# Performance work log

Hardware: AMD Instinct MI355X
Metric: run time of the kernel (lower is better)

The kernel has to match this reference:

```python
import jax, jax.numpy as jnp
import numpy as np
from jax import lax

EMB, HDIM, OBS_LEN = 64, 64, 8
BATCH, NSCENES, SCENE = 32768, 4096, 8
SEQ_LEN = 12


def setup_inputs() -> dict:
    key = jax.random.key(0)
    ks = jax.random.split(key, 16)
    obs_traj = jax.random.normal(ks[0], (OBS_LEN, BATCH, 2), jnp.float32)
    last_pos = jax.random.normal(ks[1], (BATCH, 2), jnp.float32)
    last_pos_rel = jax.random.normal(ks[2], (BATCH, 2), jnp.float32)
    starts = jnp.arange(NSCENES, dtype=jnp.int32) * SCENE
    seq_start_end = jnp.stack([starts, starts + SCENE], axis=1)  # (NSCENES, 2)
    # spatial_embedding: Linear(2, EMB)
    W_se = jax.random.normal(ks[3], (EMB, 2), jnp.float32) * 0.5
    b_se = jax.random.normal(ks[4], (EMB,), jnp.float32) * 0.1
    # weight-normed convs: w = g * v / ||v||_(in,k) per out-channel, bias init zero
    def conv_params(k, cout, cin, ksz):
        ka, kb = jax.random.split(k)
        std = np.sqrt(4.0 / (ksz * cin))
        v = jax.random.normal(ka, (cout, cin, ksz), jnp.float32) * std
        g = jax.random.uniform(kb, (cout,), jnp.float32, 0.5, 1.5)
        b = jnp.zeros((cout,), jnp.float32)
        return v, g, b
    v1, g1, b1 = conv_params(ks[5], HDIM, EMB, 3)
    v2, g2, b2 = conv_params(ks[6], HDIM // 2, HDIM, 3)
    v3, g3, b3 = conv_params(ks[7], HDIM // 2, HDIM // 2, 3)
    # hidden2pos: Linear(2*HDIM, 2)
    W_hp = jax.random.normal(ks[8], (2, 2 * HDIM), jnp.float32) * 0.05
    b_hp = jax.random.normal(ks[9], (2,), jnp.float32) * 0.05
    return {"obs_traj": obs_traj, "last_pos": last_pos, "last_pos_rel": last_pos_rel,
            "W_se": W_se, "b_se": b_se,
            "v1": v1, "g1": g1, "b1": b1,
            "v2": v2, "g2": g2, "b2": b2,
            "v3": v3, "g3": g3, "b3": b3,
            "W_hp": W_hp, "b_hp": b_hp,
            "seq_start_end": seq_start_end, "seq_len": SEQ_LEN}


def _wn_conv_relu(x, v, g, b):
    # weight-norm: w[o] = g[o] * v[o] / ||v[o]||  (norm over in-channels and kernel)
    norm = jnp.sqrt(jnp.sum(v * v, axis=(1, 2)))
    w = v * (g / norm)[:, None, None]
    y = lax.conv_general_dilated(x, w, (1,), 'VALID',
                                 dimension_numbers=('NCH', 'OIH', 'NCH'))
    return jax.nn.relu(y + b[None, :, None])


def reference(obs_traj, last_pos, last_pos_rel,
              W_se, b_se, v1, g1, b1, v2, g2, b2, v3, g3, b3, W_hp, b_hp,
              seq_start_end, seq_len):
    batch = last_pos.shape[0]
    nseg = seq_start_end.shape[0]
    h_dim = v1.shape[0]
    # scene id for each pedestrian (segments are contiguous [start,end) ranges)
    seg = jnp.searchsorted(seq_start_end[:, 0], jnp.arange(batch), side='right') - 1
    # obs_traj embedding -> (batch, EMB, OBS_LEN)
    emb = obs_traj @ W_se.T + b_se            # (T, B, EMB)
    obs_emb0 = jnp.transpose(emb, (1, 2, 0))  # (B, EMB, T)

    def step(carry, _):
        obs_emb, lp = carry
        s = _wn_conv_relu(obs_emb, v1, g1, b1)   # (B, H, T-2)
        s = _wn_conv_relu(s, v2, g2, b2)         # (B, H/2, T-4)
        s = _wn_conv_relu(s, v3, g3, b3)         # (B, H/2, T-6)
        s = s.reshape(batch, h_dim)              # (H/2)*(T-6) == H
        mx = jax.ops.segment_max(s, seg, num_segments=nseg)  # ragged per-scene max
        st = jnp.concatenate([s, mx[seg]], axis=1)           # (B, 2H)
        rel = st @ W_hp.T + b_hp                 # (B, 2)
        lp = rel + lp
        dec = rel @ W_se.T + b_se                # (B, EMB)
        obs_emb = jnp.concatenate([obs_emb[:, :, 1:], dec[:, :, None]], axis=2)
        return (obs_emb, lp), rel

    _, rels = lax.scan(step, (obs_emb0, last_pos), None, length=seq_len)
    return rels  # (seq_len, batch, 2)
```

## Files before the change

### kernel.cpp

```cpp
#include <hip/hip_runtime.h>

#define BATCH 32768
#define SEQLEN 12
#define NBLK 2048

typedef short short8 __attribute__((ext_vector_type(8)));
typedef float f32x4 __attribute__((ext_vector_type(4)));
typedef unsigned short ushort_t;

static __device__ __forceinline__ unsigned short f2bf(float x) {
    unsigned u = __float_as_uint(x);
    return (unsigned short)((u + 0x7FFFu + ((u >> 16) & 1u)) >> 16);
}
static __device__ __forceinline__ float bf2f(unsigned short h) {
    return __uint_as_float(((unsigned)h) << 16);
}

#define MFMA __builtin_amdgcn_mfma_f32_16x16x32_bf16

#define S1_FRAGREAD(SL) do {                                                  \
    __syncthreads();                                                          \
    s1fh[SL][0] = *(const short8*)&s1sh[n][kg*8];                             \
    s1fh[SL][1] = *(const short8*)&s1sh[n][32 + kg*8];                        \
    s1fl[SL][0] = *(const short8*)&s1sl[n][kg*8];                             \
    s1fl[SL][1] = *(const short8*)&s1sl[n][32 + kg*8];                        \
} while(0)

#define WCONV1(c_) do {                                                       \
    _Pragma("unroll")                                                         \
    for (int p = 0; p < 16; ++p) {                                            \
        float2 pa = *(const float2*)&pos_s[(c_)    ][p][0];                   \
        float2 pb = *(const float2*)&pos_s[(c_) + 1][p][0];                   \
        float2 pc = *(const float2*)&pos_s[(c_) + 2][p][0];                   \
        float v = cK1;                                                        \
        v = fmaf(ccA0, pa.x, v); v = fmaf(ccB0, pa.y, v);                     \
        v = fmaf(ccA1, pb.x, v); v = fmaf(ccB1, pb.y, v);                     \
        v = fmaf(ccA2, pc.x, v); v = fmaf(ccB2, pc.y, v);                     \
        v = fmaxf(v, 0.f);                                                    \
        ushort_t h = f2bf(v);                                                 \
        s1sh[p][lane] = h; s1sl[p][lane] = f2bf(v - bf2f(h));                 \
    }                                                                         \
    S1_FRAGREAD((c_) % 3);                                                    \
} while(0)

#define CONV2W(CM3) do {                                                      \
    _Pragma("unroll")                                                         \
    for (int T = 0; T < 2; ++T) {                                             \
        f32x4 a1 = {0.f,0.f,0.f,0.f}, a2 = {0.f,0.f,0.f,0.f},                 \
              a3 = {0.f,0.f,0.f,0.f};                                         \
        _Pragma("unroll")                                                     \
        for (int kb = 0; kb < 6; ++kb) {                                      \
            const int sl = ((CM3) + (kb >> 1)) % 3, ich = kb & 1;             \
            a1 = MFMA(c2h[T][kb], s1fh[sl][ich], a1, 0, 0, 0);                \
            a2 = MFMA(c2h[T][kb], s1fl[sl][ich], a2, 0, 0, 0);                \
            a3 = MFMA(c2l[T][kb], s1fh[sl][ich], a3, 0, 0, 0);                \
        }                                                                     \
        float w0 = fmaxf(a1[0]+a2[0]+a3[0]+b2r[T][0], 0.f);                   \
        float w1 = fmaxf(a1[1]+a2[1]+a3[1]+b2r[T][1], 0.f);                   \
        float w2 = fmaxf(a1[2]+a2[2]+a3[2]+b2r[T][2], 0.f);                   \
        float w3 = fmaxf(a1[3]+a2[3]+a3[3]+b2r[T][3], 0.f);                   \
        ushort_t h0=f2bf(w0), h1=f2bf(w1), h2=f2bf(w2), h3=f2bf(w3);          \
        *(uint2*)&s2sh[n][T*16 + kg*4] = make_uint2(                          \
            (unsigned)h0 | ((unsigned)h1 << 16),                              \
            (unsigned)h2 | ((unsigned)h3 << 16));                             \
        *(uint2*)&s2sl[n][T*16 + kg*4] = make_uint2(                          \
            (unsigned)f2bf(w0-bf2f(h0)) | ((unsigned)f2bf(w1-bf2f(h1)) << 16),\
            (unsigned)f2bf(w2-bf2f(h2)) | ((unsigned)f2bf(w3-bf2f(h3)) << 16));\
    }                                                                         \
    __syncthreads();                                                          \
    s2fh[(CM3)] = *(const short8*)&s2sh[n][kg*8];                             \
    s2fl[(CM3)] = *(const short8*)&s2sl[n][kg*8];                             \
} while(0)

#define CONV3W(CM3, PARI) do {                                                \
    _Pragma("unroll")                                                         \
    for (int T = 0; T < 2; ++T) {                                             \
        f32x4 a1 = {0.f,0.f,0.f,0.f}, a2 = {0.f,0.f,0.f,0.f},                 \
              a3 = {0.f,0.f,0.f,0.f};                                         \
        _Pragma("unroll")                                                     \
        for (int kb = 0; kb < 3; ++kb) {                                      \
            const int sl = ((CM3) + kb) % 3;                                  \
            a1 = MFMA(c3h[T][kb], s2fh[sl], a1, 0, 0, 0);                     \
            a2 = MFMA(c3h[T][kb], s2fl[sl], a2, 0, 0, 0);                     \
            a3 = MFMA(c3l[T][kb], s2fh[sl], a3, 0, 0, 0);                     \
        }                                                                     \
        float m0 = fmaxf(a1[0]+a2[0]+a3[0]+b3r[T][0], 0.f);                   \
        float m1 = fmaxf(a1[1]+a2[1]+a3[1]+b3r[T][1], 0.f);                   \
        float m2 = fmaxf(a1[2]+a2[2]+a3[2]+b3r[T][2], 0.f);                   \
        float m3 = fmaxf(a1[3]+a2[3]+a3[3]+b3r[T][3], 0.f);                   \
        c3c[PARI][T] = (f32x4){m0, m1, m2, m3};                               \
        _Pragma("unroll")                                                     \
        for (int msk = 1; msk <= 4; msk <<= 1) {                              \
            m0 = fmaxf(m0, __shfl_xor(m0, msk));                              \
            m1 = fmaxf(m1, __shfl_xor(m1, msk));                              \
            m2 = fmaxf(m2, __shfl_xor(m2, msk));                              \
            m3 = fmaxf(m3, __shfl_xor(m3, msk));                              \
        }                                                                     \
        mxc[PARI][T] = (f32x4){m0, m1, m2, m3};                               \
    }                                                                         \
} while(0)

#define STEP(K) do {                                                          \
    const int st = sbase + (K);                                               \
    const bool more = (st < SEQLEN-1);                                        \
    float base16[16];                                                         \
    if (more) {                                                               \
        const float* pA = &pos_s[(st+6) & 7][0][0];                           \
        const float* pB = &pos_s[(st+7) & 7][0][0];                           \
        _Pragma("unroll")                                                     \
        for (int p = 0; p < 16; ++p) {                                        \
            float v = cK1;                                                    \
            v = fmaf(ccA0, pA[p*2], v); v = fmaf(ccB0, pA[p*2+1], v);         \
            v = fmaf(ccA1, pB[p*2], v); v = fmaf(ccB1, pB[p*2+1], v);         \
            base16[p] = v;                                                    \
        }                                                                     \
    }                                                                         \
    float pv0a = 0.f, pv0b = 0.f, pv1a = 0.f, pv1b = 0.f;                     \
    {                                                                         \
        const float4* wq = (const float4*)&whp_s[kg][0];                      \
        _Pragma("unroll")                                                     \
        for (int q = 0; q < 16; ++q) {                                        \
            float4 ww = wq[q];                                                \
            _Pragma("unroll")                                                 \
            for (int e = 0; e < 4; ++e) {                                     \
                const int j2 = (q & 7)*4 + e;                                 \
                const int jj = j2 & 15;                                       \
                const int T = jj >> 3, r = (jj >> 1) & 3, col = jj & 1;       \
                const int par = col ? ((K+1) & 1) : ((K) & 1);                \
                float val = (j2 < 16) ? c3c[par][T][r] : mxc[par][T][r];      \
                float wv_ = (e==0)?ww.x:(e==1)?ww.y:(e==2)?ww.z:ww.w;         \
                if (q < 8) { if (q & 1) pv0b = fmaf(wv_, val, pv0b);          \
                             else       pv0a = fmaf(wv_, val, pv0a); }        \
                else       { if (q & 1) pv1b = fmaf(wv_, val, pv1b);          \
                             else       pv1a = fmaf(wv_, val, pv1a); }        \
            }                                                                 \
        }                                                                     \
    }                                                                         \
    float pv0 = pv0a + pv0b, pv1 = pv1a + pv1b;                               \
    pv0 += __shfl_xor(pv0, 16); pv0 += __shfl_xor(pv0, 32);                   \
    pv1 += __shfl_xor(pv1, 16); pv1 += __shfl_xor(pv1, 32);                   \
    const float r0 = pv0 + bhp0, r1 = pv1 + bhp1;                             \
    if (lane < 16) {                                                          \
        float2 o; o.x = r0; o.y = r1;                                         \
        *(float2*)&out[(size_t)(st*BATCH + bped + lane)*2] = o;               \
    }                                                                         \
    if (more) {                                                               \
        if (lane < 16) { float2 o2; o2.x = r0; o2.y = r1;                     \
            *(float2*)&pos_s[st & 7][lane][0] = o2; }                         \
        float r0g[16], r1g[16];                                               \
        _Pragma("unroll")                                                     \
        for (int p = 0; p < 16; ++p) {                                        \
            r0g[p] = __shfl(r0, p); r1g[p] = __shfl(r1, p);                   \
        }                                                                     \
        _Pragma("unroll")                                                     \
        for (int p = 0; p < 16; ++p) {                                        \
            float v = fmaf(ccB2, r1g[p], fmaf(ccA2, r0g[p], base16[p]));      \
            v = fmaxf(v, 0.f);                                                \
            ushort_t h = f2bf(v);                                             \
            s1sh[p][lane] = h; s1sl[p][lane] = f2bf(v - bf2f(h));             \
        }                                                                     \
        S1_FRAGREAD((K) % 3);            \
        CONV2W((K+1) % 3);                                      \
        CONV3W((K+2) % 3, (K) & 1);                \
    }                                                                         \
} while(0)

__global__ __launch_bounds__(64, 1)
void enc_wave(const float* __restrict__ obs,
              const float* __restrict__ Wse, const float* __restrict__ bse,
              const float* __restrict__ v1, const float* __restrict__ g1, const float* __restrict__ b1,
              const float* __restrict__ v2, const float* __restrict__ g2, const float* __restrict__ b2,
              const float* __restrict__ v3, const float* __restrict__ g3, const float* __restrict__ b3,
              const float* __restrict__ Whp, const float* __restrict__ bhp,
              float* __restrict__ out)
{
    __shared__ __align__(16) ushort_t s1sh[16][72], s1sl[16][72];
    __shared__ __align__(16) ushort_t s2sh[16][40], s2sl[16][40];
    __shared__ __align__(16) float pos_s[8][16][2];
    __shared__ __align__(16) float whp_s[4][64];
    __shared__ __align__(16) float wse_s[128], bse_s[64], sc2_s[32], sc3_s[32];

    const int lane = threadIdx.x;
    const int n = lane & 15, kg = lane >> 4;
    const int bped = blockIdx.x * 16;

    wse_s[lane] = Wse[lane]; wse_s[64 + lane] = Wse[64 + lane];
    bse_s[lane] = bse[lane];
    #pragma unroll
    for (int q = 0; q < 4; ++q) {
        int d = lane >> 5, jp = lane & 31, jj = jp & 15;
        int T = jj >> 3, r = (jj >> 1) & 3, col = jj & 1;
        int off = (T*16 + q*4 + r)*2 + col + ((jp >= 16) ? 64 : 0);
        whp_s[q][lane] = Whp[d*128 + off];
    }
    #pragma unroll
    for (int q = 0; q < 4; ++q) {
        int flat = q*64 + lane;
        int tau = flat >> 5, p = (flat >> 1) & 15, c = flat & 1;
        pos_s[tau][p][c] = obs[(size_t)(tau*BATCH + bped + p)*2 + c];
    }

    float sc1;
    {
        const float* v = v1 + lane*192; float s = 0.f;
        for (int j = 0; j < 192; ++j) s += v[j]*v[j];
        sc1 = g1[lane] / sqrtf(s);
    }
    if (lane < 32) {
        const float* v = v2 + lane*192; float s = 0.f;
        for (int j = 0; j < 192; ++j) s += v[j]*v[j];
        sc2_s[lane] = g2[lane] / sqrtf(s);
    } else {
        const float* v = v3 + (lane-32)*96; float s = 0.f;
        for (int j = 0; j < 96; ++j) s += v[j]*v[j];
        sc3_s[lane-32] = g3[lane-32] / sqrtf(s);
    }
    __syncthreads();

    float ccA0, ccA1, ccA2, ccB0, ccB1, ccB2, cK1;
    {
        float dA0=0,dA1=0,dA2=0,dB0=0,dB1=0,dB2=0,dC0=0,dC1=0,dC2=0;
        const float* vr = v1 + lane*192;
        #pragma unroll 4
        for (int ic = 0; ic < 64; ++ic) {
            float w0 = vr[ic*3], w1 = vr[ic*3+1], w2 = vr[ic*3+2];
            float we0 = wse_s[ic*2], we1 = wse_s[ic*2+1], be = bse_s[ic];
            dA0 = fmaf(w0, we0, dA0); dB0 = fmaf(w0, we1, dB0); dC0 = fmaf(w0, be, dC0);
            dA1 = fmaf(w1, we0, dA1); dB1 = fmaf(w1, we1, dB1); dC1 = fmaf(w1, be, dC1);
            dA2 = fmaf(w2, we0, dA2); dB2 = fmaf(w2, we1, dB2); dC2 = fmaf(w2, be, dC2);
        }
        ccA0 = sc1*dA0; ccA1 = sc1*dA1; ccA2 = sc1*dA2;
        ccB0 = sc1*dB0; ccB1 = sc1*dB1; ccB2 = sc1*dB2;
        float cs = (dC0 + dC1) + dC2;
        cK1 = fmaf(sc1, cs, b1[lane]);
    }

    short8 c2h[2][6], c2l[2][6], c3h[2][3], c3l[2][3];
    float b2r[2][4], b3r[2][4];
    #pragma unroll
    for (int T = 0; T < 2; ++T) {
        const int oc2 = T*16 + n;
        const float s2s = sc2_s[oc2];
        #pragma unroll
        for (int kb = 0; kb < 6; ++kb) {
            const int tap = kb >> 1, ich = kb & 1;
            #pragma unroll
            for (int j = 0; j < 8; ++j) {
                const int ic = ich*32 + kg*8 + j;
                float w = v2[(size_t)(oc2*64 + ic)*3 + tap] * s2s;
                ushort_t hb = f2bf(w);
                c2h[T][kb][j] = (short)hb;
                c2l[T][kb][j] = (short)f2bf(w - bf2f(hb));
            }
        }
        const float s3s = sc3_s[oc2];
        #pragma unroll
        for (int kb = 0; kb < 3; ++kb) {
            #pragma unroll
            for (int j = 0; j < 8; ++j) {
                const int ic = kg*8 + j;
                float w = v3[(size_t)(oc2*32 + ic)*3 + kb] * s3s;
                ushort_t hb = f2bf(w);
                c3h[T][kb][j] = (short)hb;
                c3l[T][kb][j] = (short)f2bf(w - bf2f(hb));
            }
        }
        #pragma unroll
        for (int r = 0; r < 4; ++r) {
            b2r[T][r] = b2[T*16 + kg*4 + r];
            b3r[T][r] = b3[T*16 + kg*4 + r];
        }
    }
    const float bhp0 = bhp[0], bhp1 = bhp[1];

    short8 s1fh[3][2], s1fl[3][2], s2fh[3], s2fl[3];
    f32x4 c3c[2][2], mxc[2][2];

    WCONV1(0); WCONV1(1); WCONV1(2);
    CONV2W(0);
    WCONV1(3);
    CONV2W(1);
    WCONV1(4);
    CONV2W(2);
    WCONV1(5);
    CONV3W(0, 0);
    CONV2W(0);
    CONV3W(1, 1);

    for (int hh = 0; hh < 2; ++hh) {
        const int sbase = hh * 6;
        STEP(0); STEP(1); STEP(2); STEP(3); STEP(4); STEP(5);
    }
}

extern "C" void kernel_launch(void* const* d_in, const int* in_sizes, int n_in,
                              void* d_out, int out_size, void* d_ws, size_t ws_size,
                              hipStream_t stream)
{
    const float* obs = (const float*)d_in[0];
    const float* Wse = (const float*)d_in[3];
    const float* bse = (const float*)d_in[4];
    const float* v1  = (const float*)d_in[5];
    const float* g1  = (const float*)d_in[6];
    const float* b1  = (const float*)d_in[7];
    const float* v2  = (const float*)d_in[8];
    const float* g2  = (const float*)d_in[9];
    const float* b2  = (const float*)d_in[10];
    const float* v3  = (const float*)d_in[11];
    const float* g3  = (const float*)d_in[12];
    const float* b3  = (const float*)d_in[13];
    const float* Whp = (const float*)d_in[14];
    const float* bhp = (const float*)d_in[15];

    enc_wave<<<NBLK, 64, 0, stream>>>(obs, Wse, bse, v1, g1, b1, v2, g2, b2,
                                      v3, g3, b3, Whp, bhp, (float*)d_out);
}
```

Measured before the change: 209.9 us.

## Pack four independent pedestrian waves per block and share conv3 weights in LDS

Moves from one 64-thread block per 16 pedestrians to 256-thread blocks holding four independent waves, each with private LDS slices. This amortises the weight-norm and weight-prep setup over four waves and moves conv3 weights and biases from registers into shared LDS. It also removes the per-step __syncthreads by triple-buffering conv2 outputs per wave, and recomputes the full conv1 column each step from a 4-slot position ring instead of precomputing partial sums. The costs are extra LDS traffic for conv3 weights, a larger LDS footprint, and recomputed conv1 work.

New measurement: 206.9 us. No clear change (-1.4%).

```diff
diff --git a/kernel.cpp b/kernel.cpp
--- a/kernel.cpp
+++ b/kernel.cpp
@@ -2,7 +2,7 @@
 
 #define BATCH 32768
 #define SEQLEN 12
-#define NBLK 2048
+#define NBLK 512
 
 typedef short short8 __attribute__((ext_vector_type(8)));
 typedef float f32x4 __attribute__((ext_vector_type(4)));
@@ -18,32 +18,38 @@
 
 #define MFMA __builtin_amdgcn_mfma_f32_16x16x32_bf16
 
+
+#define C1PED(PX, PY, QX, QY, RX, RY, PPED) do {                              \
+    float v_ = cK1;                                                           \
+    v_ = fmaf(ccA0, PX, v_); v_ = fmaf(ccB0, PY, v_);                         \
+    v_ = fmaf(ccA1, QX, v_); v_ = fmaf(ccB1, QY, v_);                         \
+    v_ = fmaf(ccA2, RX, v_); v_ = fmaf(ccB2, RY, v_);                         \
+    v_ = fmaxf(v_, 0.f);                                                      \
+    ushort_t h_ = f2bf(v_);                                                   \
+    s1sh[wv][PPED][lane] = h_;                                                \
+    s1sl[wv][PPED][lane] = f2bf(v_ - bf2f(h_));                               \
+} while(0)
+
 #define S1_FRAGREAD(SL) do {                                                  \
-    __syncthreads();                                                          \
-    s1fh[SL][0] = *(const short8*)&s1sh[n][kg*8];                             \
-    s1fh[SL][1] = *(const short8*)&s1sh[n][32 + kg*8];                        \
-    s1fl[SL][0] = *(const short8*)&s1sl[n][kg*8];                             \
-    s1fl[SL][1] = *(const short8*)&s1sl[n][32 + kg*8];                        \
-} while(0)
-
-#define WCONV1(c_) do {                                                       \
+    s1fh[SL][0] = *(const short8*)&s1sh[wv][n][kg*8];                         \
+    s1fh[SL][1] = *(const short8*)&s1sh[wv][n][32 + kg*8];                    \
+    s1fl[SL][0] = *(const short8*)&s1sl[wv][n][kg*8];                         \
+    s1fl[SL][1] = *(const short8*)&s1sl[wv][n][32 + kg*8];                    \
+} while(0)
+
+#define CONV1COL(SA, SB, SC, SL) do {                                         \
     _Pragma("unroll")                                                         \
-    for (int p = 0; p < 16; ++p) {                                            \
-        float2 pa = *(const float2*)&pos_s[(c_)    ][p][0];                   \
-        float2 pb = *(const float2*)&pos_s[(c_) + 1][p][0];                   \
-        float2 pc = *(const float2*)&pos_s[(c_) + 2][p][0];                   \
-        float v = cK1;                                                        \
-        v = fmaf(ccA0, pa.x, v); v = fmaf(ccB0, pa.y, v);                     \
-        v = fmaf(ccA1, pb.x, v); v = fmaf(ccB1, pb.y, v);                     \
-        v = fmaf(ccA2, pc.x, v); v = fmaf(ccB2, pc.y, v);                     \
-        v = fmaxf(v, 0.f);                                                    \
-        ushort_t h = f2bf(v);                                                 \
-        s1sh[p][lane] = h; s1sl[p][lane] = f2bf(v - bf2f(h));                 \
-    }                                                                         \
-    S1_FRAGREAD((c_) % 3);                                                    \
-} while(0)
-
-#define CONV2W(CM3) do {                                                      \
+    for (int pp_ = 0; pp_ < 8; ++pp_) {                                       \
+        float4 fa_ = *(const float4*)&pos_s[wv][SA][2*pp_][0];                \
+        float4 fb_ = *(const float4*)&pos_s[wv][SB][2*pp_][0];                \
+        float4 fc_ = *(const float4*)&pos_s[wv][SC][2*pp_][0];                \
+        C1PED(fa_.x, fa_.y, fb_.x, fb_.y, fc_.x, fc_.y, 2*pp_);               \
+        C1PED(fa_.z, fa_.w, fb_.z, fb_.w, fc_.z, fc_.w, 2*pp_+1);             \
+    }                                                                         \
+    S1_FRAGREAD(SL);                                                          \
+} while(0)
+
+#define CONV2COL(CM3) do {                                                    \
     _Pragma("unroll")                                                         \
     for (int T = 0; T < 2; ++T) {                                             \
         f32x4 a1 = {0.f,0.f,0.f,0.f}, a2 = {0.f,0.f,0.f,0.f},                 \
@@ -55,39 +61,46 @@
             a2 = MFMA(c2h[T][kb], s1fl[sl][ich], a2, 0, 0, 0);                \
             a3 = MFMA(c2l[T][kb], s1fh[sl][ich], a3, 0, 0, 0);                \
         }                                                                     \
-        float w0 = fmaxf(a1[0]+a2[0]+a3[0]+b2r[T][0], 0.f);                   \
-        float w1 = fmaxf(a1[1]+a2[1]+a3[1]+b2r[T][1], 0.f);                   \
-        float w2 = fmaxf(a1[2]+a2[2]+a3[2]+b2r[T][2], 0.f);                   \
-        float w3 = fmaxf(a1[3]+a2[3]+a3[3]+b2r[T][3], 0.f);                   \
+        const float4 bb = *(const float4*)&b2s[T*16 + kg*4];                  \
+        float w0 = fmaxf(a1[0]+a2[0]+a3[0]+bb.x, 0.f);                        \
+        float w1 = fmaxf(a1[1]+a2[1]+a3[1]+bb.y, 0.f);                        \
+        float w2 = fmaxf(a1[2]+a2[2]+a3[2]+bb.z, 0.f);                        \
+        float w3 = fmaxf(a1[3]+a2[3]+a3[3]+bb.w, 0.f);                        \
         ushort_t h0=f2bf(w0), h1=f2bf(w1), h2=f2bf(w2), h3=f2bf(w3);          \
-        *(uint2*)&s2sh[n][T*16 + kg*4] = make_uint2(                          \
+        *(uint2*)&s2sh[wv][CM3][n][T*16 + kg*4] = make_uint2(                 \
             (unsigned)h0 | ((unsigned)h1 << 16),                              \
             (unsigned)h2 | ((unsigned)h3 << 16));                             \
-        *(uint2*)&s2sl[n][T*16 + kg*4] = make_uint2(                          \
+        *(uint2*)&s2sl[wv][CM3][n][T*16 + kg*4] = make_uint2(                 \
             (unsigned)f2bf(w0-bf2f(h0)) | ((unsigned)f2bf(w1-bf2f(h1)) << 16),\
             (unsigned)f2bf(w2-bf2f(h2)) | ((unsigned)f2bf(w3-bf2f(h3)) << 16));\
     }                                                                         \
-    __syncthreads();                                                          \
-    s2fh[(CM3)] = *(const short8*)&s2sh[n][kg*8];                             \
-    s2fl[(CM3)] = *(const short8*)&s2sl[n][kg*8];                             \
-} while(0)
-
-#define CONV3W(CM3, PARI) do {                                                \
+} while(0)
+
+#define CONV3COL(VM3, PARI) do {                                              \
+    short8 sbh_[3], sbl_[3];                                                  \
+    _Pragma("unroll")                                                         \
+    for (int kb = 0; kb < 3; ++kb) {                                          \
+        const int sl = ((VM3) + kb) % 3;                                      \
+        sbh_[kb] = *(const short8*)&s2sh[wv][sl][n][kg*8];                    \
+        sbl_[kb] = *(const short8*)&s2sl[wv][sl][n][kg*8];                    \
+    }                                                                         \
     _Pragma("unroll")                                                         \
     for (int T = 0; T < 2; ++T) {                                             \
         f32x4 a1 = {0.f,0.f,0.f,0.f}, a2 = {0.f,0.f,0.f,0.f},                 \
               a3 = {0.f,0.f,0.f,0.f};                                         \
         _Pragma("unroll")                                                     \
         for (int kb = 0; kb < 3; ++kb) {                                      \
-            const int sl = ((CM3) + kb) % 3;                                  \
-            a1 = MFMA(c3h[T][kb], s2fh[sl], a1, 0, 0, 0);                     \
-            a2 = MFMA(c3h[T][kb], s2fl[sl], a2, 0, 0, 0);                     \
-            a3 = MFMA(c3l[T][kb], s2fh[sl], a3, 0, 0, 0);                     \
-        }                                                                     \
-        float m0 = fmaxf(a1[0]+a2[0]+a3[0]+b3r[T][0], 0.f);                   \
-        float m1 = fmaxf(a1[1]+a2[1]+a3[1]+b3r[T][1], 0.f);                   \
-        float m2 = fmaxf(a1[2]+a2[2]+a3[2]+b3r[T][2], 0.f);                   \
-        float m3 = fmaxf(a1[3]+a2[3]+a3[3]+b3r[T][3], 0.f);                   \
+            const short8 wh = *(const short8*)&c3wh[T*3+kb][lane][0];         \
+            const short8 wl = *(const short8*)&c3wl[T*3+kb][lane][0];         \
+            a1 = MFMA(wh, sbh_[kb], a1, 0, 0, 0);                             \
+            a2 = MFMA(wh, sbl_[kb], a2, 0, 0, 0);                             \
+            a3 = MFMA(wl, sbh_[kb], a3, 0, 0, 0);                             \
+        }                                                                     \
+        const float4 b3v = *(const float4*)&b3s[T*16 + kg*4];                 \
+        float m0 = fmaxf(a1[0]+a2[0]+a3[0]+b3v.x, 0.f);                       \
+        float m1 = fmaxf(a1[1]+a2[1]+a3[1]+b3v.y, 0.f);                       \
+        float m2 = fmaxf(a1[2]+a2[2]+a3[2]+b3v.z, 0.f);                       \
+        float m3 = fmaxf(a1[3]+a2[3]+a3[3]+b3v.w, 0.f);                       \
         c3c[PARI][T] = (f32x4){m0, m1, m2, m3};                               \
         _Pragma("unroll")                                                     \
         for (int msk = 1; msk <= 4; msk <<= 1) {                              \
@@ -100,21 +113,15 @@
     }                                                                         \
 } while(0)
 
+#define STAGE2(T0) do {                                                       \
+    const int tau_ = (T0) + (lane >> 5);                                      \
+    const int p_ = (lane >> 1) & 15, c_ = lane & 1;                           \
+    pos_s[wv][tau_ & 3][p_][c_] =                                             \
+        obs[(size_t)(tau_*BATCH + bped + p_)*2 + c_];                         \
+} while(0)
+
 #define STEP(K) do {                                                          \
     const int st = sbase + (K);                                               \
-    const bool more = (st < SEQLEN-1);                                        \
-    float base16[16];                                                         \
-    if (more) {                                                               \
-        const float* pA = &pos_s[(st+6) & 7][0][0];                           \
-        const float* pB = &pos_s[(st+7) & 7][0][0];                           \
-        _Pragma("unroll")                                                     \
-        for (int p = 0; p < 16; ++p) {                                        \
-            float v = cK1;                                                    \
-            v = fmaf(ccA0, pA[p*2], v); v = fmaf(ccB0, pA[p*2+1], v);         \
-            v = fmaf(ccA1, pB[p*2], v); v = fmaf(ccB1, pB[p*2+1], v);         \
-            base16[p] = v;                                                    \
-        }                                                                     \
-    }                                                                         \
     float pv0a = 0.f, pv0b = 0.f, pv1a = 0.f, pv1b = 0.f;                     \
     {                                                                         \
         const float4* wq = (const float4*)&whp_s[kg][0];                      \
@@ -126,7 +133,7 @@
                 const int j2 = (q & 7)*4 + e;                                 \
                 const int jj = j2 & 15;                                       \
                 const int T = jj >> 3, r = (jj >> 1) & 3, col = jj & 1;       \
-                const int par = col ? ((K+1) & 1) : ((K) & 1);                \
+                const int par = col ? (((K)+1) & 1) : ((K) & 1);              \
                 float val = (j2 < 16) ? c3c[par][T][r] : mxc[par][T][r];      \
                 float wv_ = (e==0)?ww.x:(e==1)?ww.y:(e==2)?ww.z:ww.w;         \
                 if (q < 8) { if (q & 1) pv0b = fmaf(wv_, val, pv0b);          \
@@ -144,81 +151,74 @@
         float2 o; o.x = r0; o.y = r1;                                         \
         *(float2*)&out[(size_t)(st*BATCH + bped + lane)*2] = o;               \
     }                                                                         \
-    if (more) {                                                               \
-        if (lane < 16) { float2 o2; o2.x = r0; o2.y = r1;                     \
-            *(float2*)&pos_s[st & 7][lane][0] = o2; }                         \
-        float r0g[16], r1g[16];                                               \
-        _Pragma("unroll")                                                     \
-        for (int p = 0; p < 16; ++p) {                                        \
-            r0g[p] = __shfl(r0, p); r1g[p] = __shfl(r1, p);                   \
-        }                                                                     \
-        _Pragma("unroll")                                                     \
-        for (int p = 0; p < 16; ++p) {                                        \
-            float v = fmaf(ccB2, r1g[p], fmaf(ccA2, r0g[p], base16[p]));      \
-            v = fmaxf(v, 0.f);                                                \
-            ushort_t h = f2bf(v);                                             \
-            s1sh[p][lane] = h; s1sl[p][lane] = f2bf(v - bf2f(h));             \
-        }                                                                     \
-        S1_FRAGREAD((K) % 3);            \
-        CONV2W((K+1) % 3);                                      \
-        CONV3W((K+2) % 3, (K) & 1);                \
-    }                                                                         \
-} while(0)
-
-__global__ __launch_bounds__(64, 1)
-void enc_wave(const float* __restrict__ obs,
-              const float* __restrict__ Wse, const float* __restrict__ bse,
-              const float* __restrict__ v1, const float* __restrict__ g1, const float* __restrict__ b1,
-              const float* __restrict__ v2, const float* __restrict__ g2, const float* __restrict__ b2,
-              const float* __restrict__ v3, const float* __restrict__ g3, const float* __restrict__ b3,
-              const float* __restrict__ Whp, const float* __restrict__ bhp,
-              float* __restrict__ out)
+    if (st < SEQLEN-1) {                                                      \
+        if (lane < 16) {                                                      \
+            float2 o2; o2.x = r0; o2.y = r1;                                  \
+            *(float2*)&pos_s[wv][st & 3][lane][0] = o2;         \
+        }                                                                     \
+        CONV1COL((st+2)&3, (st+3)&3, st&3, (K)%3);              \
+        CONV2COL(((K)+1)%3);                                    \
+        CONV3COL(((K)+2)%3, (K)&1);                             \
+    }                                                                         \
+} while(0)
+
+__global__ __launch_bounds__(256, 1)
+void enc_wp(const float* __restrict__ obs,
+            const float* __restrict__ Wse, const float* __restrict__ bse,
+            const float* __restrict__ v1, const float* __restrict__ g1, const float* __restrict__ b1,
+            const float* __restrict__ v2, const float* __restrict__ g2, const float* __restrict__ b2,
+            const float* __restrict__ v3, const float* __restrict__ g3, const float* __restrict__ b3,
+            const float* __restrict__ Whp, const float* __restrict__ bhp,
+            float* __restrict__ out)
 {
-    __shared__ __align__(16) ushort_t s1sh[16][72], s1sl[16][72];
-    __shared__ __align__(16) ushort_t s2sh[16][40], s2sl[16][40];
-    __shared__ __align__(16) float pos_s[8][16][2];
-    __shared__ __align__(16) float whp_s[4][64];
-    __shared__ __align__(16) float wse_s[128], bse_s[64], sc2_s[32], sc3_s[32];
-
-    const int lane = threadIdx.x;
-    const int n = lane & 15, kg = lane >> 4;
-    const int bped = blockIdx.x * 16;
-
-    wse_s[lane] = Wse[lane]; wse_s[64 + lane] = Wse[64 + lane];
-    bse_s[lane] = bse[lane];
-    #pragma unroll
-    for (int q = 0; q < 4; ++q) {
-        int d = lane >> 5, jp = lane & 31, jj = jp & 15;
-        int T = jj >> 3, r = (jj >> 1) & 3, col = jj & 1;
-        int off = (T*16 + q*4 + r)*2 + col + ((jp >= 16) ? 64 : 0);
-        whp_s[q][lane] = Whp[d*128 + off];
-    }
-    #pragma unroll
-    for (int q = 0; q < 4; ++q) {
-        int flat = q*64 + lane;
-        int tau = flat >> 5, p = (flat >> 1) & 15, c = flat & 1;
-        pos_s[tau][p][c] = obs[(size_t)(tau*BATCH + bped + p)*2 + c];
-    }
-
-    float sc1;
+    __shared__ __align__(16) ushort_t s1sh[4][16][72], s1sl[4][16][72];
+    __shared__ __align__(16) ushort_t s2sh[4][3][16][40], s2sl[4][3][16][40];
+    __shared__ __align__(16) float    pos_s[4][4][16][2];
+    __shared__ __align__(16) float    whp_s[4][68];
+    __shared__ __align__(16) ushort_t c3wh[6][64][8], c3wl[6][64][8];
+    __shared__ __align__(16) float    b2s[32], b3s[32];
+
+    const int tid  = threadIdx.x;
+    const int wv   = tid >> 6;
+    const int lane = tid & 63;
+    const int n    = lane & 15, kg = lane >> 4;
+    const int bped = (blockIdx.x*4 + wv)*16;
+
+    float* scr   = (float*)&s2sh[0][0][0][0];
+    float* wse_s = scr;
+    float* bse_s = scr + 128;
+    float* sc2_s = scr + 192;
+    float* sc3_s = scr + 224;
+
+    if (wv == 0) {
+        wse_s[lane] = Wse[lane]; wse_s[64 + lane] = Wse[64 + lane];
+        bse_s[lane] = bse[lane];
+        if (lane < 32) {
+            b2s[lane] = b2[lane];
+            const float* v = v2 + lane*192; float s = 0.f;
+            for (int j = 0; j < 192; ++j) s += v[j]*v[j];
+            sc2_s[lane] = g2[lane] / sqrtf(s);
+        } else {
+            b3s[lane-32] = b3[lane-32];
+            const float* v = v3 + (lane-32)*96; float s = 0.f;
+            for (int j = 0; j < 96; ++j) s += v[j]*v[j];
+            sc3_s[lane-32] = g3[lane-32] / sqrtf(s);
+        }
+        #pragma unroll
+        for (int q = 0; q < 4; ++q) {
+            int d = lane >> 5, jp = lane & 31, jj = jp & 15;
+            int T = jj >> 3, r = (jj >> 1) & 3, col = jj & 1;
+            int off = (T*16 + q*4 + r)*2 + col + ((jp >= 16) ? 64 : 0);
+            whp_s[q][lane] = Whp[d*128 + off];
+        }
+    }
+    __syncthreads();
+
+    float ccA0, ccA1, ccA2, ccB0, ccB1, ccB2, cK1;
     {
         const float* v = v1 + lane*192; float s = 0.f;
         for (int j = 0; j < 192; ++j) s += v[j]*v[j];
-        sc1 = g1[lane] / sqrtf(s);
-    }
-    if (lane < 32) {
-        const float* v = v2 + lane*192; float s = 0.f;
-        for (int j = 0; j < 192; ++j) s += v[j]*v[j];
-        sc2_s[lane] = g2[lane] / sqrtf(s);
-    } else {
-        const float* v = v3 + (lane-32)*96; float s = 0.f;
-        for (int j = 0; j < 96; ++j) s += v[j]*v[j];
-        sc3_s[lane-32] = g3[lane-32] / sqrtf(s);
-    }
-    __syncthreads();
-
-    float ccA0, ccA1, ccA2, ccB0, ccB1, ccB2, cK1;
-    {
+        const float sc1 = g1[lane] / sqrtf(s);
         float dA0=0,dA1=0,dA2=0,dB0=0,dB1=0,dB2=0,dC0=0,dC1=0,dC2=0;
         const float* vr = v1 + lane*192;
         #pragma unroll 4
@@ -231,12 +231,9 @@
         }
         ccA0 = sc1*dA0; ccA1 = sc1*dA1; ccA2 = sc1*dA2;
         ccB0 = sc1*dB0; ccB1 = sc1*dB1; ccB2 = sc1*dB2;
-        float cs = (dC0 + dC1) + dC2;
-        cK1 = fmaf(sc1, cs, b1[lane]);
-    }
-
-    short8 c2h[2][6], c2l[2][6], c3h[2][3], c3l[2][3];
-    float b2r[2][4], b3r[2][4];
+        cK1  = fmaf(sc1, (dC0 + dC1) + dC2, b1[lane]);
+    }
+    short8 c2h[2][6], c2l[2][6];
     #pragma unroll
     for (int T = 0; T < 2; ++T) {
         const int oc2 = T*16 + n;
@@ -253,40 +250,46 @@
                 c2l[T][kb][j] = (short)f2bf(w - bf2f(hb));
             }
         }
-        const float s3s = sc3_s[oc2];
+    }
+    if (wv == 1) {
         #pragma unroll
-        for (int kb = 0; kb < 3; ++kb) {
+        for (int f = 0; f < 6; ++f) {
+            const int T = f / 3, kb = f % 3;
+            const int oc = T*16 + n;
+            const float s3s = sc3_s[oc];
             #pragma unroll
             for (int j = 0; j < 8; ++j) {
                 const int ic = kg*8 + j;
-                float w = v3[(size_t)(oc2*32 + ic)*3 + kb] * s3s;
+                float w = v3[(size_t)(oc*32 + ic)*3 + kb] * s3s;
                 ushort_t hb = f2bf(w);
-                c3h[T][kb][j] = (short)hb;
-                c3l[T][kb][j] = (short)f2bf(w - bf2f(hb));
+                c3wh[f][lane][j] = hb;
+                c3wl[f][lane][j] = f2bf(w - bf2f(hb));
             }
         }
-        #pragma unroll
-        for (int r = 0; r < 4; ++r) {
-            b2r[T][r] = b2[T*16 + kg*4 + r];
-            b3r[T][r] = b3[T*16 + kg*4 + r];
-        }
     }
     const float bhp0 = bhp[0], bhp1 = bhp[1];
-
-    short8 s1fh[3][2], s1fl[3][2], s2fh[3], s2fl[3];
+    __syncthreads();
+
+    short8 s1fh[3][2], s1fl[3][2];
     f32x4 c3c[2][2], mxc[2][2];
 
-    WCONV1(0); WCONV1(1); WCONV1(2);
-    CONV2W(0);
-    WCONV1(3);
-    CONV2W(1);
-    WCONV1(4);
-    CONV2W(2);
-    WCONV1(5);
-    CONV3W(0, 0);
-    CONV2W(0);
-    CONV3W(1, 1);
-
+    STAGE2(0); STAGE2(2);
+    CONV1COL(0, 1, 2, 0);
+    CONV1COL(1, 2, 3, 1);
+    STAGE2(4);
+    CONV1COL(2, 3, 0, 2);
+    CONV2COL(0);
+    CONV1COL(3, 0, 1, 0);
+    CONV2COL(1);
+    STAGE2(6);
+    CONV1COL(0, 1, 2, 1);
+    CONV2COL(2);
+    CONV3COL(0, 0);
+    CONV1COL(1, 2, 3, 2);
+    CONV2COL(0);
+    CONV3COL(1, 1);
+
+    #pragma unroll 1
     for (int hh = 0; hh < 2; ++hh) {
         const int sbase = hh * 6;
         STEP(0); STEP(1); STEP(2); STEP(3); STEP(4); STEP(5);
@@ -312,6 +315,6 @@
     const float* Whp = (const float*)d_in[14];
     const float* bhp = (const float*)d_in[15];
 
-    enc_wave<<<NBLK, 64, 0, stream>>>(obs, Wse, bse, v1, g1, b1, v2, g2, b2,
-                                      v3, g3, b3, Whp, bhp, (float*)d_out);
+    enc_wp<<<NBLK, 256, 0, stream>>>(obs, Wse, bse, v1, g1, b1, v2, g2, b2,
+                                     v3, g3, b3, Whp, bhp, (float*)d_out);
 }
```
